# Kernel tuning notes

Hardware: AMD Instinct MI355X
Metric: run time of the kernel (lower is better)

Reference implementation:

```python
import jax, jax.numpy as jnp
import numpy as np

N_NODES = 100000
N_EDGES = 1600000
IN_CH = 128
HID = 128
OUT_CH = 10
NUM_LAYERS = 3
NUM_GRAPHS = 512


def _glorot(key, shape):
    fan_in, fan_out = shape[0], shape[1]
    lim = jnp.sqrt(6.0 / (fan_in + fan_out))
    return jax.random.uniform(key, shape, jnp.float32, -lim, lim)


def setup_inputs() -> dict:
    key = jax.random.key(0)
    ks = jax.random.split(key, 20)
    inp = {}
    inp["x"] = jax.random.normal(ks[0], (N_NODES, IN_CH), jnp.float32)
    inp["edge_index"] = jax.random.randint(ks[1], (2, N_EDGES), 0, N_NODES, jnp.int64)
    inp["batch"] = jnp.sort(jax.random.randint(ks[2], (N_NODES,), 0, NUM_GRAPHS, jnp.int64))
    # GIN layer MLP params: Linear(in, hid) -> ReLU -> Linear(hid, hid)
    kidx = 3
    for l in range(NUM_LAYERS):
        d_in = IN_CH if l == 0 else HID
        inp[f"w1_{l}"] = _glorot(ks[kidx], (d_in, HID)); kidx += 1
        inp[f"b1_{l}"] = jnp.zeros((HID,), jnp.float32)
        inp[f"w2_{l}"] = _glorot(ks[kidx], (HID, HID)); kidx += 1
        inp[f"b2_{l}"] = jnp.zeros((HID,), jnp.float32)
    inp["lin_w"] = _glorot(ks[kidx], (HID, OUT_CH))
    inp["lin_b"] = jnp.zeros((OUT_CH,), jnp.float32)
    return inp


def _gin_forward(x, src, dst, batch, layer_params, lin_w, lin_b):
    h = x
    n_layers = len(layer_params)
    for i, (w1, b1, w2, b2) in enumerate(layer_params):
        # GINConv: (1 + eps) * h + sum_{j in N(i)} h_j, eps = 0
        agg = jax.ops.segment_sum(h[src], dst, num_segments=N_NODES)
        z = h + agg
        # MLP: Linear -> ReLU -> Linear
        h = jnp.maximum(z @ w1 + b1, 0.0) @ w2 + b2
        if i < n_layers - 1:  # inter-layer ReLU (PyG BasicGNN act)
            h = jnp.maximum(h, 0.0)
    # global_add_pool over batch ids -> [NUM_GRAPHS, HID]
    pooled = jax.ops.segment_sum(h, batch, num_segments=NUM_GRAPHS)
    # dropout(p=0.5) is identity in eval mode
    return pooled @ lin_w + lin_b


def reference(x, edge_index, batch,
              w1_0, b1_0, w2_0, b2_0,
              w1_1, b1_1, w2_1, b2_1,
              w1_2, b1_2, w2_2, b2_2,
              lin_w, lin_b):
    src, dst = edge_index[0], edge_index[1]
    layer_params = [(w1_0, b1_0, w2_0, b2_0),
                    (w1_1, b1_1, w2_1, b2_1),
                    (w1_2, b1_2, w2_2, b2_2)]
    return _gin_forward(x, src, dst, batch, layer_params, lin_w, lin_b)
```

## Files before the change

### kernel.cpp

```cpp
#include <hip/hip_runtime.h>

#define CH 128
#define OUTC 10
#define NB 256
#define BCAP 10240
#define PCHUNK 2048

typedef __attribute__((ext_vector_type(8))) short short8;
typedef __attribute__((ext_vector_type(4))) short short4v;
typedef __attribute__((ext_vector_type(16))) float f32x16;


__device__ inline unsigned short f2bf(float f) {
    unsigned u = __builtin_bit_cast(unsigned, f);
    u += 0x7fffu + ((u >> 16) & 1u);
    return (unsigned short)(u >> 16);
}
__device__ inline float bflo(unsigned u) { return __builtin_bit_cast(float, u << 16); }
__device__ inline float bfhi(unsigned u) { return __builtin_bit_cast(float, u & 0xffff0000u); }

__device__ inline void acc8(float* a, const uint4& v) {
    a[0] += bflo(v.x); a[1] += bfhi(v.x);
    a[2] += bflo(v.y); a[3] += bfhi(v.y);
    a[4] += bflo(v.z); a[5] += bfhi(v.z);
    a[6] += bflo(v.w); a[7] += bfhi(v.w);
}


struct WPtrs { const float* s[6]; unsigned short* d[6]; };

__global__ void prep_kernel(const float4* __restrict__ x4, uint2* __restrict__ xb, int n4,
                            int nConvBlk, WPtrs p) {
    int tid = threadIdx.x;
    if ((int)blockIdx.x < nConvBlk) {
        int i = blockIdx.x * 256 + tid;
        if (i < n4) {
            float4 v = x4[i];
            uint2 o;
            o.x = (unsigned)f2bf(v.x) | ((unsigned)f2bf(v.y) << 16);
            o.y = (unsigned)f2bf(v.z) | ((unsigned)f2bf(v.w) << 16);
            xb[i] = o;
        }
    } else {
        int b = blockIdx.x - nConvBlk;
        int m = b >> 6;
        int i = (b & 63) * 256 + tid;
        int j = i & 7;
        int l = (i >> 3) & 63;
        int k0 = (i >> 9) & 7;
        int ct = (i >> 12) & 3;
        int k = k0 * 16 + ((l >> 5) << 3) + j;
        int nn = ct * 32 + (l & 31);
        p.d[m][i] = f2bf(p.s[m][k * CH + nn]);
    }
}


__global__ void partition_kernel(const int* __restrict__ src, const int* __restrict__ dst,
                                 int* __restrict__ bucketCnt, unsigned* __restrict__ pairs, int E) {
    __shared__ int hist[NB];
    __shared__ int base[NB];
    __shared__ int cur[NB];
    int tid = threadIdx.x;
    int e0 = blockIdx.x * PCHUNK;

    hist[tid] = 0;
    __syncthreads();
    #pragma unroll
    for (int i = 0; i < PCHUNK / 256; ++i) {
        int e = e0 + tid + i * 256;
        if (e < E) atomicAdd(&hist[dst[e] >> 9], 1);
    }
    __syncthreads();
    {
        int c = hist[tid];
        base[tid] = (c > 0) ? atomicAdd(&bucketCnt[tid], c) : 0;
        cur[tid] = 0;
    }
    __syncthreads();
    #pragma unroll
    for (int i = 0; i < PCHUNK / 256; ++i) {
        int e = e0 + tid + i * 256;
        if (e < E) {
            int d = dst[e];
            int bkt = d >> 9;
            int p = base[bkt] + atomicAdd(&cur[bkt], 1);
            if (p < BCAP)
                pairs[bkt * BCAP + p] = ((unsigned)(d & 511) << 17) | (unsigned)src[e];
        }
    }
}


__launch_bounds__(256)
__global__ void build_csr_kernel(const unsigned* __restrict__ pairs, const int* __restrict__ bucketCnt,
                                 int* __restrict__ offs, int* __restrict__ csr, int N) {
    __shared__ int bsm[NB];
    __shared__ int ldeg[512];
    __shared__ int s0[512], s1[512];
    __shared__ int lexc[512];
    __shared__ int lcur[512];
    __shared__ int lcsr[BCAP];

    int b = blockIdx.x;
    int node0 = b << 9;
    if (node0 >= N) return;
    int nLocal = min(512, N - node0);
    int tid = threadIdx.x;

    bsm[tid] = bucketCnt[tid];
    __syncthreads();
    for (int off = 1; off < NB; off <<= 1) {
        int t = (tid >= off) ? bsm[tid - off] : 0;
        __syncthreads();
        bsm[tid] += t;
        __syncthreads();
    }
    int cnt = min(bucketCnt[b], BCAP);
    int gbase = bsm[b] - bucketCnt[b];

    for (int i = tid; i < 512; i += 256) ldeg[i] = 0;
    __syncthreads();
    for (int i = tid; i < cnt; i += 256)
        atomicAdd(&ldeg[pairs[b * BCAP + i] >> 17], 1);
    __syncthreads();

    for (int i = tid; i < 512; i += 256) s0[i] = ldeg[i];
    __syncthreads();
    int* sp = s0; int* dp = s1;
    for (int off = 1; off < 512; off <<= 1) {
        for (int i = tid; i < 512; i += 256)
            dp[i] = sp[i] + ((i >= off) ? sp[i - off] : 0);
        __syncthreads();
        int* t = sp; sp = dp; dp = t;
    }
    for (int i = tid; i < 512; i += 256) {
        int ex = sp[i] - ldeg[i];
        lexc[i] = ex;
        lcur[i] = ex;
    }
    __syncthreads();

    for (int i = tid; i < cnt; i += 256) {
        unsigned w = pairs[b * BCAP + i];
        int ppos = atomicAdd(&lcur[w >> 17], 1);
        lcsr[ppos] = (int)(w & 0x1ffffu);
    }
    __syncthreads();

    for (int i = tid; i < cnt; i += 256) csr[gbase + i] = lcsr[i];
    for (int i = tid; i < nLocal; i += 256) offs[node0 + i] = gbase + lexc[i];
    if (tid == 0 && node0 + nLocal == N) offs[N] = gbase + cnt;
}


template <int L>
__global__ void aggregate_kernel(const uint4* __restrict__ h4, const int* __restrict__ offs,
                                 const int* __restrict__ csr, uint4* __restrict__ z4, int n) {
    int node = blockIdx.x * 16 + (threadIdx.x >> 4);
    int lane = threadIdx.x & 15;
    if (node >= n) return;
    int beg = offs[node], end = offs[node + 1];

    float a[8];
    {
        uint4 self = h4[node * 16 + lane];
        a[0] = bflo(self.x); a[1] = bfhi(self.x);
        a[2] = bflo(self.y); a[3] = bfhi(self.y);
        a[4] = bflo(self.z); a[5] = bfhi(self.z);
        a[6] = bflo(self.w); a[7] = bfhi(self.w);
    }
    int e = beg;
    for (; e + 4 <= end; e += 4) {
        int s0 = csr[e], s1 = csr[e + 1], s2 = csr[e + 2], s3 = csr[e + 3];
        uint4 v0 = h4[s0 * 16 + lane];
        uint4 v1 = h4[s1 * 16 + lane];
        uint4 v2 = h4[s2 * 16 + lane];
        uint4 v3 = h4[s3 * 16 + lane];
        acc8(a, v0); acc8(a, v1); acc8(a, v2); acc8(a, v3);
    }
    for (; e < end; ++e) {
        uint4 v = h4[csr[e] * 16 + lane];
        acc8(a, v);
    }
    uint4 o;
    o.x = (unsigned)f2bf(a[0]) | ((unsigned)f2bf(a[1]) << 16);
    o.y = (unsigned)f2bf(a[2]) | ((unsigned)f2bf(a[3]) << 16);
    o.z = (unsigned)f2bf(a[4]) | ((unsigned)f2bf(a[5]) << 16);
    o.w = (unsigned)f2bf(a[6]) | ((unsigned)f2bf(a[7]) << 16);
    z4[node * 16 + lane] = o;
}


#define PQ2 132
#define BM 128

template <int L, int RELU, int POOL>
__launch_bounds__(512)
__global__ void mlp_mfma_kernel(const unsigned short* __restrict__ z,
                                const unsigned short* __restrict__ w1s, const float* __restrict__ b1,
                                const unsigned short* __restrict__ w2s, const float* __restrict__ b2,
                                unsigned short* __restrict__ hout,
                                const int* __restrict__ batch, float* __restrict__ pooled,
                                int n) {
    __shared__ __align__(16) unsigned short zs[BM * PQ2];

    int tid = threadIdx.x;
    int row0 = blockIdx.x * BM;
    int wv = tid >> 6;
    int lane = tid & 63;
    int l31 = lane & 31;
    int kh = lane >> 5;
    int rt = wv & 3;
    int ch = wv >> 2;
    int ct0 = ch * 2;
    int arow = rt * 32 + l31;

    for (int i = tid; i < BM * 16; i += 512) {
        int r = i >> 4, c = i & 15;
        int row = row0 + r;
        uint4 v = (row < n) ? ((const uint4*)z)[row * 16 + c] : make_uint4(0, 0, 0, 0);
        *(uint2*)&zs[r * PQ2 + c * 8]     = make_uint2(v.x, v.y);
        *(uint2*)&zs[r * PQ2 + c * 8 + 4] = make_uint2(v.z, v.w);
    }
    __syncthreads();

    f32x16 acc0, acc1;
    {
        float bv0 = b1[ct0 * 32 + l31];
        float bv1 = b1[(ct0 + 1) * 32 + l31];
        #pragma unroll
        for (int r = 0; r < 16; ++r) { acc0[r] = bv0; acc1[r] = bv1; }
    }
    #pragma unroll
    for (int k0 = 0; k0 < 8; ++k0) {
        short8 afr;
        {
            short4v lo = *(const short4v*)&zs[arow * PQ2 + k0 * 16 + kh * 8];
            short4v hi = *(const short4v*)&zs[arow * PQ2 + k0 * 16 + kh * 8 + 4];
            afr = (short8){lo[0], lo[1], lo[2], lo[3], hi[0], hi[1], hi[2], hi[3]};
        }
        short8 bf0 = *(const short8*)&w1s[(((ct0 * 8 + k0) * 64) + lane) * 8];
        short8 bf1 = *(const short8*)&w1s[((((ct0 + 1) * 8 + k0) * 64) + lane) * 8];
        acc0 = __builtin_amdgcn_mfma_f32_32x32x16_bf16(afr, bf0, acc0, 0, 0, 0);
        acc1 = __builtin_amdgcn_mfma_f32_32x32x16_bf16(afr, bf1, acc1, 0, 0, 0);
    }
    __syncthreads();

    #pragma unroll
    for (int reg = 0; reg < 16; ++reg) {
        int crow = (reg & 3) + 8 * (reg >> 2) + 4 * kh;
        zs[(rt * 32 + crow) * PQ2 + ch * 64 + l31]      = f2bf(fmaxf(acc0[reg], 0.f));
        zs[(rt * 32 + crow) * PQ2 + ch * 64 + 32 + l31] = f2bf(fmaxf(acc1[reg], 0.f));
    }
    __syncthreads();

    {
        float bv0 = b2[ct0 * 32 + l31];
        float bv1 = b2[(ct0 + 1) * 32 + l31];
        #pragma unroll
        for (int r = 0; r < 16; ++r) { acc0[r] = bv0; acc1[r] = bv1; }
    }
    #pragma unroll
    for (int k0 = 0; k0 < 8; ++k0) {
        short8 afr;
        {
            short4v lo = *(const short4v*)&zs[arow * PQ2 + k0 * 16 + kh * 8];
            short4v hi = *(const short4v*)&zs[arow * PQ2 + k0 * 16 + kh * 8 + 4];
            afr = (short8){lo[0], lo[1], lo[2], lo[3], hi[0], hi[1], hi[2], hi[3]};
        }
        short8 bf0 = *(const short8*)&w2s[(((ct0 * 8 + k0) * 64) + lane) * 8];
        short8 bf1 = *(const short8*)&w2s[((((ct0 + 1) * 8 + k0) * 64) + lane) * 8];
        acc0 = __builtin_amdgcn_mfma_f32_32x32x16_bf16(afr, bf0, acc0, 0, 0, 0);
        acc1 = __builtin_amdgcn_mfma_f32_32x32x16_bf16(afr, bf1, acc1, 0, 0, 0);
    }
    __syncthreads();

    #pragma unroll
    for (int reg = 0; reg < 16; ++reg) {
        int crow = (reg & 3) + 8 * (reg >> 2) + 4 * kh;
        float v0 = acc0[reg], v1 = acc1[reg];
        if (RELU) { v0 = fmaxf(v0, 0.f); v1 = fmaxf(v1, 0.f); }
        zs[(rt * 32 + crow) * PQ2 + ch * 64 + l31]      = f2bf(v0);
        zs[(rt * 32 + crow) * PQ2 + ch * 64 + 32 + l31] = f2bf(v1);
    }
    __syncthreads();

    if (!POOL) {
        for (int i = tid; i < BM * 16; i += 512) {
            int r = i >> 4, c = i & 15;
            int row = row0 + r;
            if (row < n) {
                uint2 a = *(const uint2*)&zs[r * PQ2 + c * 8];
                uint2 b = *(const uint2*)&zs[r * PQ2 + c * 8 + 4];
                ((uint4*)hout)[row * 16 + c] = make_uint4(a.x, a.y, b.x, b.y);
            }
        }
    } else {
        int c2 = tid & 63;
        int rs = tid >> 6;
        float a0 = 0.f, a1 = 0.f;
        int prevg = -1;
        #pragma unroll
        for (int i = 0; i < BM / 8; ++i) {
            int r = rs + 8 * i;
            int row = row0 + r;
            if (row >= n) break;
            int g = batch[row];
            if (g != prevg) {
                if (prevg >= 0) {
                    atomicAdd(&pooled[prevg * CH + 2 * c2], a0);
                    atomicAdd(&pooled[prevg * CH + 2 * c2 + 1], a1);
                }
                prevg = g; a0 = 0.f; a1 = 0.f;
            }
            unsigned v = *(const unsigned*)&zs[r * PQ2 + c2 * 2];
            a0 += bflo(v); a1 += bfhi(v);
        }
        if (prevg >= 0) {
            atomicAdd(&pooled[prevg * CH + 2 * c2], a0);
            atomicAdd(&pooled[prevg * CH + 2 * c2 + 1], a1);
        }
    }
}


__global__ void final_linear_kernel(const float* __restrict__ pooled, const float* __restrict__ lin_w,
                                    const float* __restrict__ lin_b, float* __restrict__ out) {
    int g = blockIdx.x;
    int tid = threadIdx.x;
    __shared__ float pl[CH];
    pl[tid] = pooled[g * CH + tid];
    __syncthreads();
    if (tid < OUTC) {
        float a = lin_b[tid];
        #pragma unroll 16
        for (int c = 0; c < CH; ++c) a = fmaf(pl[c], lin_w[c * OUTC + tid], a);
        out[g * OUTC + tid] = a;
    }
}


static inline size_t aln(size_t x) { return (x + 255) & ~size_t(255); }

extern "C" void kernel_launch(void* const* d_in, const int* in_sizes, int n_in,
                              void* d_out, int out_size, void* d_ws, size_t ws_size,
                              hipStream_t stream) {
    const float* x      = (const float*)d_in[0];
    const int*   ei     = (const int*)d_in[1];
    const int*   batch  = (const int*)d_in[2];
    const float* w1[3]  = {(const float*)d_in[3], (const float*)d_in[7],  (const float*)d_in[11]};
    const float* b1[3]  = {(const float*)d_in[4], (const float*)d_in[8],  (const float*)d_in[12]};
    const float* w2[3]  = {(const float*)d_in[5], (const float*)d_in[9],  (const float*)d_in[13]};
    const float* b2[3]  = {(const float*)d_in[6], (const float*)d_in[10], (const float*)d_in[14]};
    const float* lin_w  = (const float*)d_in[15];
    const float* lin_b  = (const float*)d_in[16];
    float* out = (float*)d_out;

    int E = in_sizes[1] / 2;
    int N = in_sizes[2];
    int n_graphs = out_size / OUTC;
    const int* src = ei;
    const int* dst = ei + E;

    char* p = (char*)d_ws;
    int* bucketCnt  = (int*)p; p += aln(NB * 4);
    unsigned* pairs = (unsigned*)p; p += aln((size_t)NB * BCAP * 4);
    int* offs       = (int*)p; p += aln((size_t)(N + 1) * 4);
    int* csr        = (int*)p; p += aln((size_t)E * 4);
    unsigned short* xb = (unsigned short*)p; p += aln((size_t)N * CH * 2);
    unsigned short* zb = (unsigned short*)p; p += aln((size_t)N * CH * 2);
    unsigned short* hA = (unsigned short*)p; p += aln((size_t)N * CH * 2);
    unsigned short* hB = (unsigned short*)p; p += aln((size_t)N * CH * 2);
    float* pooled = (float*)p; p += aln((size_t)n_graphs * CH * 4);
    unsigned short* wt[6];
    for (int i = 0; i < 6; ++i) { wt[i] = (unsigned short*)p; p += aln((size_t)CH * CH * 2); }
    (void)ws_size; (void)n_in;

    hipMemsetAsync(bucketCnt, 0, NB * 4, stream);
    hipMemsetAsync(pooled, 0, (size_t)n_graphs * CH * 4, stream);

    int n4 = N * CH / 4;
    int nConvBlk = (n4 + 255) / 256;
    WPtrs wp;
    for (int l = 0; l < 3; ++l) {
        wp.s[2 * l] = w1[l];     wp.d[2 * l] = wt[2 * l];
        wp.s[2 * l + 1] = w2[l]; wp.d[2 * l + 1] = wt[2 * l + 1];
    }
    prep_kernel<<<nConvBlk + 384, 256, 0, stream>>>((const float4*)x, (uint2*)xb, n4, nConvBlk, wp);

    partition_kernel<<<(E + PCHUNK - 1) / PCHUNK, 256, 0, stream>>>(src, dst, bucketCnt, pairs, E);
    build_csr_kernel<<<NB, 256, 0, stream>>>(pairs, bucketCnt, offs, csr, N);

    int ablk = (N + 15) / 16;
    int mblk = (N + BM - 1) / BM;

    aggregate_kernel<0><<<ablk, 256, 0, stream>>>((const uint4*)xb, offs, csr, (uint4*)zb, N);
    mlp_mfma_kernel<0, 1, 0><<<mblk, 512, 0, stream>>>(zb, wt[0], b1[0], wt[1], b2[0], hA, batch, pooled, N);
    aggregate_kernel<1><<<ablk, 256, 0, stream>>>((const uint4*)hA, offs, csr, (uint4*)zb, N);
    mlp_mfma_kernel<1, 1, 0><<<mblk, 512, 0, stream>>>(zb, wt[2], b1[1], wt[3], b2[1], hB, batch, pooled, N);
    aggregate_kernel<2><<<ablk, 256, 0, stream>>>((const uint4*)hB, offs, csr, (uint4*)zb, N);
    mlp_mfma_kernel<2, 0, 1><<<mblk, 512, 0, stream>>>(zb, wt[4], b1[2], wt[5], b2[2], hA, batch, pooled, N);

    final_linear_kernel<<<n_graphs, CH, 0, stream>>>(pooled, lin_w, lin_b, out);
}
```

Measured before the change: 435.3 us.

## Fuse layer-1 aggregation with MLP and fold memsets into prep kernel

Adds a fused kernel that gathers neighbor features for a 64-row tile straight into shared memory and then runs both MFMA linear layers on that tile, so the bf16 z buffer is never written to or read back from global memory for layer 1. The two hipMemsetAsync calls are also replaced by extra blocks in the prep kernel that zero the bucket counts and the pooled buffer, cutting two launches. The fused kernel uses 512 threads per 64-row block, which may lower occupancy or the gather's memory parallelism compared with the separate aggregate kernel. Layers 0 and 2 still use the unfused path.

```diff
diff --git a/kernel.cpp b/kernel.cpp
--- a/kernel.cpp
+++ b/kernel.cpp
@@ -30,10 +30,12 @@
 struct WPtrs { const float* s[6]; unsigned short* d[6]; };
 
 __global__ void prep_kernel(const float4* __restrict__ x4, uint2* __restrict__ xb, int n4,
-                            int nConvBlk, WPtrs p) {
+                            int nConvBlk, WPtrs p, int* __restrict__ bucketCnt,
+                            uint4* __restrict__ pooled4, int nPooled4) {
     int tid = threadIdx.x;
-    if ((int)blockIdx.x < nConvBlk) {
-        int i = blockIdx.x * 256 + tid;
+    int b = blockIdx.x;
+    if (b < nConvBlk) {
+        int i = b * 256 + tid;
         if (i < n4) {
             float4 v = x4[i];
             uint2 o;
@@ -41,10 +43,10 @@
             o.y = (unsigned)f2bf(v.z) | ((unsigned)f2bf(v.w) << 16);
             xb[i] = o;
         }
-    } else {
-        int b = blockIdx.x - nConvBlk;
-        int m = b >> 6;
-        int i = (b & 63) * 256 + tid;
+    } else if (b < nConvBlk + 384) {
+        int bb = b - nConvBlk;
+        int m = bb >> 6;
+        int i = (bb & 63) * 256 + tid;
         int j = i & 7;
         int l = (i >> 3) & 63;
         int k0 = (i >> 9) & 7;
@@ -52,6 +54,11 @@
         int k = k0 * 16 + ((l >> 5) << 3) + j;
         int nn = ct * 32 + (l & 31);
         p.d[m][i] = f2bf(p.s[m][k * CH + nn]);
+    } else if (b == nConvBlk + 384) {
+        bucketCnt[tid] = 0;
+    } else {
+        int i = (b - nConvBlk - 385) * 256 + tid;
+        if (i < nPooled4) pooled4[i] = make_uint4(0, 0, 0, 0);
     }
 }
 
@@ -191,8 +198,9 @@
     z4[node * 16 + lane] = o;
 }
 
-
 #define PQ2 132
+
+
 #define BM 128
 
 template <int L, int RELU, int POOL>
@@ -325,6 +333,133 @@
 }
 
 
+#define FBM 64
+
+template <int RELU>
+__launch_bounds__(512)
+__global__ void fused_gin_kernel(const uint4* __restrict__ h4,
+                                 const int* __restrict__ offs, const int* __restrict__ csr,
+                                 const unsigned short* __restrict__ w1s, const float* __restrict__ b1,
+                                 const unsigned short* __restrict__ w2s, const float* __restrict__ b2,
+                                 unsigned short* __restrict__ hout, int n) {
+    __shared__ __align__(16) unsigned short zs[FBM * PQ2];
+
+    int tid = threadIdx.x;
+    int row0 = blockIdx.x * FBM;
+
+    {
+        int gl = tid & 15;
+        int grp = tid >> 4;
+        #pragma unroll
+        for (int it = 0; it < 2; ++it) {
+            int rr = grp + 32 * it;
+            int node = row0 + rr;
+            unsigned o0 = 0, o1 = 0, o2 = 0, o3 = 0;
+            if (node < n) {
+                int beg = offs[node], end = offs[node + 1];
+                float a[8];
+                uint4 self = h4[node * 16 + gl];
+                a[0] = bflo(self.x); a[1] = bfhi(self.x);
+                a[2] = bflo(self.y); a[3] = bfhi(self.y);
+                a[4] = bflo(self.z); a[5] = bfhi(self.z);
+                a[6] = bflo(self.w); a[7] = bfhi(self.w);
+                int e = beg;
+                for (; e + 4 <= end; e += 4) {
+                    int s0 = csr[e], s1 = csr[e + 1], s2 = csr[e + 2], s3 = csr[e + 3];
+                    uint4 v0 = h4[s0 * 16 + gl];
+                    uint4 v1 = h4[s1 * 16 + gl];
+                    uint4 v2 = h4[s2 * 16 + gl];
+                    uint4 v3 = h4[s3 * 16 + gl];
+                    acc8(a, v0); acc8(a, v1); acc8(a, v2); acc8(a, v3);
+                }
+                for (; e < end; ++e) {
+                    uint4 v = h4[csr[e] * 16 + gl];
+                    acc8(a, v);
+                }
+                o0 = (unsigned)f2bf(a[0]) | ((unsigned)f2bf(a[1]) << 16);
+                o1 = (unsigned)f2bf(a[2]) | ((unsigned)f2bf(a[3]) << 16);
+                o2 = (unsigned)f2bf(a[4]) | ((unsigned)f2bf(a[5]) << 16);
+                o3 = (unsigned)f2bf(a[6]) | ((unsigned)f2bf(a[7]) << 16);
+            }
+            *(uint2*)&zs[rr * PQ2 + gl * 8]     = make_uint2(o0, o1);
+            *(uint2*)&zs[rr * PQ2 + gl * 8 + 4] = make_uint2(o2, o3);
+        }
+    }
+    __syncthreads();
+
+    int wv = tid >> 6;
+    int lane = tid & 63;
+    int l31 = lane & 31;
+    int kh = lane >> 5;
+    int rt = wv & 1;
+    int ct = wv >> 1;
+    int arow = rt * 32 + l31;
+
+    f32x16 acc;
+    {
+        float bv = b1[ct * 32 + l31];
+        #pragma unroll
+        for (int r = 0; r < 16; ++r) acc[r] = bv;
+    }
+    #pragma unroll
+    for (int k0 = 0; k0 < 8; ++k0) {
+        short8 afr;
+        {
+            short4v lo = *(const short4v*)&zs[arow * PQ2 + k0 * 16 + kh * 8];
+            short4v hi = *(const short4v*)&zs[arow * PQ2 + k0 * 16 + kh * 8 + 4];
+            afr = (short8){lo[0], lo[1], lo[2], lo[3], hi[0], hi[1], hi[2], hi[3]};
+        }
+        short8 bfr = *(const short8*)&w1s[(((ct * 8 + k0) * 64) + lane) * 8];
+        acc = __builtin_amdgcn_mfma_f32_32x32x16_bf16(afr, bfr, acc, 0, 0, 0);
+    }
+    __syncthreads();
+
+    #pragma unroll
+    for (int reg = 0; reg < 16; ++reg) {
+        int crow = (reg & 3) + 8 * (reg >> 2) + 4 * kh;
+        zs[(rt * 32 + crow) * PQ2 + ct * 32 + l31] = f2bf(fmaxf(acc[reg], 0.f));
+    }
+    __syncthreads();
+
+    {
+        float bv = b2[ct * 32 + l31];
+        #pragma unroll
+        for (int r = 0; r < 16; ++r) acc[r] = bv;
+    }
+    #pragma unroll
+    for (int k0 = 0; k0 < 8; ++k0) {
+        short8 afr;
+        {
+            short4v lo = *(const short4v*)&zs[arow * PQ2 + k0 * 16 + kh * 8];
+            short4v hi = *(const short4v*)&zs[arow * PQ2 + k0 * 16 + kh * 8 + 4];
+            afr = (short8){lo[0], lo[1], lo[2], lo[3], hi[0], hi[1], hi[2], hi[3]};
+        }
+        short8 bfr = *(const short8*)&w2s[(((ct * 8 + k0) * 64) + lane) * 8];
+        acc = __builtin_amdgcn_mfma_f32_32x32x16_bf16(afr, bfr, acc, 0, 0, 0);
+    }
+    __syncthreads();
+
+    #pragma unroll
+    for (int reg = 0; reg < 16; ++reg) {
+        int crow = (reg & 3) + 8 * (reg >> 2) + 4 * kh;
+        float v = acc[reg];
+        if (RELU) v = fmaxf(v, 0.f);
+        zs[(rt * 32 + crow) * PQ2 + ct * 32 + l31] = f2bf(v);
+    }
+    __syncthreads();
+
+    for (int i = tid; i < FBM * 16; i += 512) {
+        int r = i >> 4, c = i & 15;
+        int row = row0 + r;
+        if (row < n) {
+            uint2 a = *(const uint2*)&zs[r * PQ2 + c * 8];
+            uint2 b = *(const uint2*)&zs[r * PQ2 + c * 8 + 4];
+            ((uint4*)hout)[row * 16 + c] = make_uint4(a.x, a.y, b.x, b.y);
+        }
+    }
+}
+
+
 __global__ void final_linear_kernel(const float* __restrict__ pooled, const float* __restrict__ lin_w,
                                     const float* __restrict__ lin_b, float* __restrict__ out) {
     int g = blockIdx.x;
@@ -377,28 +512,29 @@
     for (int i = 0; i < 6; ++i) { wt[i] = (unsigned short*)p; p += aln((size_t)CH * CH * 2); }
     (void)ws_size; (void)n_in;
 
-    hipMemsetAsync(bucketCnt, 0, NB * 4, stream);
-    hipMemsetAsync(pooled, 0, (size_t)n_graphs * CH * 4, stream);
-
     int n4 = N * CH / 4;
     int nConvBlk = (n4 + 255) / 256;
+    int nPooled4 = n_graphs * CH / 4;
+    int nZeroBlk = (nPooled4 + 255) / 256;
     WPtrs wp;
     for (int l = 0; l < 3; ++l) {
         wp.s[2 * l] = w1[l];     wp.d[2 * l] = wt[2 * l];
         wp.s[2 * l + 1] = w2[l]; wp.d[2 * l + 1] = wt[2 * l + 1];
     }
-    prep_kernel<<<nConvBlk + 384, 256, 0, stream>>>((const float4*)x, (uint2*)xb, n4, nConvBlk, wp);
+    prep_kernel<<<nConvBlk + 384 + 1 + nZeroBlk, 256, 0, stream>>>(
+        (const float4*)x, (uint2*)xb, n4, nConvBlk, wp, bucketCnt, (uint4*)pooled, nPooled4);
 
     partition_kernel<<<(E + PCHUNK - 1) / PCHUNK, 256, 0, stream>>>(src, dst, bucketCnt, pairs, E);
     build_csr_kernel<<<NB, 256, 0, stream>>>(pairs, bucketCnt, offs, csr, N);
 
     int ablk = (N + 15) / 16;
     int mblk = (N + BM - 1) / BM;
+    int fblk = (N + FBM - 1) / FBM;
 
     aggregate_kernel<0><<<ablk, 256, 0, stream>>>((const uint4*)xb, offs, csr, (uint4*)zb, N);
     mlp_mfma_kernel<0, 1, 0><<<mblk, 512, 0, stream>>>(zb, wt[0], b1[0], wt[1], b2[0], hA, batch, pooled, N);
-    aggregate_kernel<1><<<ablk, 256, 0, stream>>>((const uint4*)hA, offs, csr, (uint4*)zb, N);
-    mlp_mfma_kernel<1, 1, 0><<<mblk, 512, 0, stream>>>(zb, wt[2], b1[1], wt[3], b2[1], hB, batch, pooled, N);
+    fused_gin_kernel<1><<<fblk, 512, 0, stream>>>((const uint4*)hA, offs, csr,
+                                                  wt[2], b1[1], wt[3], b2[1], hB, N);
     aggregate_kernel<2><<<ablk, 256, 0, stream>>>((const uint4*)hB, offs, csr, (uint4*)zb, N);
     mlp_mfma_kernel<2, 0, 1><<<mblk, 512, 0, stream>>>(zb, wt[4], b1[2], wt[5], b2[2], hA, batch, pooled, N);
 
```

Result: faster. 412.2 us (-5.3%).

## Fuse neighbor aggregation into MLP kernel and merge prep, partition, pool-zero launches

Applied to the files above, without the earlier changes.

The gather-sum aggregation is moved into the MFMA MLP kernel, so each 64-row block builds its z tile directly in shared memory and the z buffer never makes a round trip through global memory. The M tile shrinks from 128 to 64 rows, with each wave now owning a single 32-column tile. Partitioning, input conversion, weight swizzle and zeroing of the pooled buffer are merged into one launch, removing a memset and a kernel launch. In exchange, the MLP phase waits on irregular gather latency inside each block, and per-wave MFMA work is smaller.

```diff
diff --git a/kernel.cpp b/kernel.cpp
--- a/kernel.cpp
+++ b/kernel.cpp
@@ -5,6 +5,8 @@
 #define NB 256
 #define BCAP 10240
 #define PCHUNK 2048
+#define PQ2 132
+#define FBM 64
 
 typedef __attribute__((ext_vector_type(8))) short short8;
 typedef __attribute__((ext_vector_type(4))) short short4v;
@@ -29,11 +31,47 @@
 
 struct WPtrs { const float* s[6]; unsigned short* d[6]; };
 
-__global__ void prep_kernel(const float4* __restrict__ x4, uint2* __restrict__ xb, int n4,
-                            int nConvBlk, WPtrs p) {
+__global__ void prep_part_kernel(const int* __restrict__ src, const int* __restrict__ dst,
+                                 int* __restrict__ bucketCnt, unsigned* __restrict__ pairs, int E,
+                                 int nPartBlk,
+                                 const float4* __restrict__ x4, uint2* __restrict__ xb, int n4,
+                                 int nConvBlk, WPtrs p,
+                                 uint4* __restrict__ pooled4, int nPooled4) {
+    __shared__ int hist[NB];
+    __shared__ int base[NB];
+    __shared__ int cur[NB];
     int tid = threadIdx.x;
-    if ((int)blockIdx.x < nConvBlk) {
-        int i = blockIdx.x * 256 + tid;
+    int b = blockIdx.x;
+
+    if (b < nPartBlk) {
+        int e0 = b * PCHUNK;
+        hist[tid] = 0;
+        __syncthreads();
+        #pragma unroll
+        for (int i = 0; i < PCHUNK / 256; ++i) {
+            int e = e0 + tid + i * 256;
+            if (e < E) atomicAdd(&hist[dst[e] >> 9], 1);
+        }
+        __syncthreads();
+        {
+            int c = hist[tid];
+            base[tid] = (c > 0) ? atomicAdd(&bucketCnt[tid], c) : 0;
+            cur[tid] = 0;
+        }
+        __syncthreads();
+        #pragma unroll
+        for (int i = 0; i < PCHUNK / 256; ++i) {
+            int e = e0 + tid + i * 256;
+            if (e < E) {
+                int d = dst[e];
+                int bkt = d >> 9;
+                int pos = base[bkt] + atomicAdd(&cur[bkt], 1);
+                if (pos < BCAP)
+                    pairs[bkt * BCAP + pos] = ((unsigned)(d & 511) << 17) | (unsigned)src[e];
+            }
+        }
+    } else if (b < nPartBlk + nConvBlk) {
+        int i = (b - nPartBlk) * 256 + tid;
         if (i < n4) {
             float4 v = x4[i];
             uint2 o;
@@ -41,10 +79,10 @@
             o.y = (unsigned)f2bf(v.z) | ((unsigned)f2bf(v.w) << 16);
             xb[i] = o;
         }
-    } else {
-        int b = blockIdx.x - nConvBlk;
-        int m = b >> 6;
-        int i = (b & 63) * 256 + tid;
+    } else if (b < nPartBlk + nConvBlk + 384) {
+        int bb = b - nPartBlk - nConvBlk;
+        int m = bb >> 6;
+        int i = (bb & 63) * 256 + tid;
         int j = i & 7;
         int l = (i >> 3) & 63;
         int k0 = (i >> 9) & 7;
@@ -52,42 +90,9 @@
         int k = k0 * 16 + ((l >> 5) << 3) + j;
         int nn = ct * 32 + (l & 31);
         p.d[m][i] = f2bf(p.s[m][k * CH + nn]);
-    }
-}
-
-
-__global__ void partition_kernel(const int* __restrict__ src, const int* __restrict__ dst,
-                                 int* __restrict__ bucketCnt, unsigned* __restrict__ pairs, int E) {
-    __shared__ int hist[NB];
-    __shared__ int base[NB];
-    __shared__ int cur[NB];
-    int tid = threadIdx.x;
-    int e0 = blockIdx.x * PCHUNK;
-
-    hist[tid] = 0;
-    __syncthreads();
-    #pragma unroll
-    for (int i = 0; i < PCHUNK / 256; ++i) {
-        int e = e0 + tid + i * 256;
-        if (e < E) atomicAdd(&hist[dst[e] >> 9], 1);
-    }
-    __syncthreads();
-    {
-        int c = hist[tid];
-        base[tid] = (c > 0) ? atomicAdd(&bucketCnt[tid], c) : 0;
-        cur[tid] = 0;
-    }
-    __syncthreads();
-    #pragma unroll
-    for (int i = 0; i < PCHUNK / 256; ++i) {
-        int e = e0 + tid + i * 256;
-        if (e < E) {
-            int d = dst[e];
-            int bkt = d >> 9;
-            int p = base[bkt] + atomicAdd(&cur[bkt], 1);
-            if (p < BCAP)
-                pairs[bkt * BCAP + p] = ((unsigned)(d & 511) << 17) | (unsigned)src[e];
-        }
+    } else {
+        int i = (b - nPartBlk - nConvBlk - 384) * 256 + tid;
+        if (i < nPooled4) pooled4[i] = make_uint4(0, 0, 0, 0);
     }
 }
 
@@ -154,83 +159,73 @@
 }
 
 
-template <int L>
-__global__ void aggregate_kernel(const uint4* __restrict__ h4, const int* __restrict__ offs,
-                                 const int* __restrict__ csr, uint4* __restrict__ z4, int n) {
-    int node = blockIdx.x * 16 + (threadIdx.x >> 4);
-    int lane = threadIdx.x & 15;
-    if (node >= n) return;
-    int beg = offs[node], end = offs[node + 1];
-
-    float a[8];
-    {
-        uint4 self = h4[node * 16 + lane];
-        a[0] = bflo(self.x); a[1] = bfhi(self.x);
-        a[2] = bflo(self.y); a[3] = bfhi(self.y);
-        a[4] = bflo(self.z); a[5] = bfhi(self.z);
-        a[6] = bflo(self.w); a[7] = bfhi(self.w);
-    }
-    int e = beg;
-    for (; e + 4 <= end; e += 4) {
-        int s0 = csr[e], s1 = csr[e + 1], s2 = csr[e + 2], s3 = csr[e + 3];
-        uint4 v0 = h4[s0 * 16 + lane];
-        uint4 v1 = h4[s1 * 16 + lane];
-        uint4 v2 = h4[s2 * 16 + lane];
-        uint4 v3 = h4[s3 * 16 + lane];
-        acc8(a, v0); acc8(a, v1); acc8(a, v2); acc8(a, v3);
-    }
-    for (; e < end; ++e) {
-        uint4 v = h4[csr[e] * 16 + lane];
-        acc8(a, v);
-    }
-    uint4 o;
-    o.x = (unsigned)f2bf(a[0]) | ((unsigned)f2bf(a[1]) << 16);
-    o.y = (unsigned)f2bf(a[2]) | ((unsigned)f2bf(a[3]) << 16);
-    o.z = (unsigned)f2bf(a[4]) | ((unsigned)f2bf(a[5]) << 16);
-    o.w = (unsigned)f2bf(a[6]) | ((unsigned)f2bf(a[7]) << 16);
-    z4[node * 16 + lane] = o;
-}
-
-
-#define PQ2 132
-#define BM 128
-
 template <int L, int RELU, int POOL>
 __launch_bounds__(512)
-__global__ void mlp_mfma_kernel(const unsigned short* __restrict__ z,
-                                const unsigned short* __restrict__ w1s, const float* __restrict__ b1,
-                                const unsigned short* __restrict__ w2s, const float* __restrict__ b2,
-                                unsigned short* __restrict__ hout,
-                                const int* __restrict__ batch, float* __restrict__ pooled,
-                                int n) {
-    __shared__ __align__(16) unsigned short zs[BM * PQ2];
+__global__ void fused_gin_kernel(const uint4* __restrict__ h4,
+                                 const int* __restrict__ offs, const int* __restrict__ csr,
+                                 const unsigned short* __restrict__ w1s, const float* __restrict__ b1,
+                                 const unsigned short* __restrict__ w2s, const float* __restrict__ b2,
+                                 unsigned short* __restrict__ hout,
+                                 const int* __restrict__ batch, float* __restrict__ pooled,
+                                 int n) {
+    __shared__ __align__(16) unsigned short zs[FBM * PQ2];
 
     int tid = threadIdx.x;
-    int row0 = blockIdx.x * BM;
+    int row0 = blockIdx.x * FBM;
+
+    {
+        int gl = tid & 15;
+        int grp = tid >> 4;
+        #pragma unroll
+        for (int it = 0; it < 2; ++it) {
+            int rr = grp + 32 * it;
+            int node = row0 + rr;
+            unsigned o0 = 0, o1 = 0, o2 = 0, o3 = 0;
+            if (node < n) {
+                int beg = offs[node], end = offs[node + 1];
+                float a[8];
+                uint4 self = h4[node * 16 + gl];
+                a[0] = bflo(self.x); a[1] = bfhi(self.x);
+                a[2] = bflo(self.y); a[3] = bfhi(self.y);
+                a[4] = bflo(self.z); a[5] = bfhi(self.z);
+                a[6] = bflo(self.w); a[7] = bfhi(self.w);
+                int e = beg;
+                for (; e + 4 <= end; e += 4) {
+                    int s0 = csr[e], s1 = csr[e + 1], s2 = csr[e + 2], s3 = csr[e + 3];
+                    uint4 v0 = h4[s0 * 16 + gl];
+                    uint4 v1 = h4[s1 * 16 + gl];
+                    uint4 v2 = h4[s2 * 16 + gl];
+                    uint4 v3 = h4[s3 * 16 + gl];
+                    acc8(a, v0); acc8(a, v1); acc8(a, v2); acc8(a, v3);
+                }
+                for (; e < end; ++e) {
+                    uint4 v = h4[csr[e] * 16 + gl];
+                    acc8(a, v);
+                }
+                o0 = (unsigned)f2bf(a[0]) | ((unsigned)f2bf(a[1]) << 16);
+                o1 = (unsigned)f2bf(a[2]) | ((unsigned)f2bf(a[3]) << 16);
+                o2 = (unsigned)f2bf(a[4]) | ((unsigned)f2bf(a[5]) << 16);
+                o3 = (unsigned)f2bf(a[6]) | ((unsigned)f2bf(a[7]) << 16);
+            }
+            *(uint2*)&zs[rr * PQ2 + gl * 8]     = make_uint2(o0, o1);
+            *(uint2*)&zs[rr * PQ2 + gl * 8 + 4] = make_uint2(o2, o3);
+        }
+    }
+    __syncthreads();
+
     int wv = tid >> 6;
     int lane = tid & 63;
     int l31 = lane & 31;
     int kh = lane >> 5;
-    int rt = wv & 3;
-    int ch = wv >> 2;
-    int ct0 = ch * 2;
+    int rt = wv & 1;
+    int ct = wv >> 1;
     int arow = rt * 32 + l31;
 
-    for (int i = tid; i < BM * 16; i += 512) {
-        int r = i >> 4, c = i & 15;
-        int row = row0 + r;
-        uint4 v = (row < n) ? ((const uint4*)z)[row * 16 + c] : make_uint4(0, 0, 0, 0);
-        *(uint2*)&zs[r * PQ2 + c * 8]     = make_uint2(v.x, v.y);
-        *(uint2*)&zs[r * PQ2 + c * 8 + 4] = make_uint2(v.z, v.w);
-    }
-    __syncthreads();
-
-    f32x16 acc0, acc1;
+    f32x16 acc;
     {
-        float bv0 = b1[ct0 * 32 + l31];
-        float bv1 = b1[(ct0 + 1) * 32 + l31];
-        #pragma unroll
-        for (int r = 0; r < 16; ++r) { acc0[r] = bv0; acc1[r] = bv1; }
+        float bv = b1[ct * 32 + l31];
+        #pragma unroll
+        for (int r = 0; r < 16; ++r) acc[r] = bv;
     }
     #pragma unroll
     for (int k0 = 0; k0 < 8; ++k0) {
@@ -240,26 +235,22 @@
             short4v hi = *(const short4v*)&zs[arow * PQ2 + k0 * 16 + kh * 8 + 4];
             afr = (short8){lo[0], lo[1], lo[2], lo[3], hi[0], hi[1], hi[2], hi[3]};
         }
-        short8 bf0 = *(const short8*)&w1s[(((ct0 * 8 + k0) * 64) + lane) * 8];
-        short8 bf1 = *(const short8*)&w1s[((((ct0 + 1) * 8 + k0) * 64) + lane) * 8];
-        acc0 = __builtin_amdgcn_mfma_f32_32x32x16_bf16(afr, bf0, acc0, 0, 0, 0);
-        acc1 = __builtin_amdgcn_mfma_f32_32x32x16_bf16(afr, bf1, acc1, 0, 0, 0);
+        short8 bfr = *(const short8*)&w1s[(((ct * 8 + k0) * 64) + lane) * 8];
+        acc = __builtin_amdgcn_mfma_f32_32x32x16_bf16(afr, bfr, acc, 0, 0, 0);
     }
     __syncthreads();
 
     #pragma unroll
     for (int reg = 0; reg < 16; ++reg) {
         int crow = (reg & 3) + 8 * (reg >> 2) + 4 * kh;
-        zs[(rt * 32 + crow) * PQ2 + ch * 64 + l31]      = f2bf(fmaxf(acc0[reg], 0.f));
-        zs[(rt * 32 + crow) * PQ2 + ch * 64 + 32 + l31] = f2bf(fmaxf(acc1[reg], 0.f));
+        zs[(rt * 32 + crow) * PQ2 + ct * 32 + l31] = f2bf(fmaxf(acc[reg], 0.f));
     }
     __syncthreads();
 
     {
-        float bv0 = b2[ct0 * 32 + l31];
-        float bv1 = b2[(ct0 + 1) * 32 + l31];
-        #pragma unroll
-        for (int r = 0; r < 16; ++r) { acc0[r] = bv0; acc1[r] = bv1; }
+        float bv = b2[ct * 32 + l31];
+        #pragma unroll
+        for (int r = 0; r < 16; ++r) acc[r] = bv;
     }
     #pragma unroll
     for (int k0 = 0; k0 < 8; ++k0) {
@@ -269,25 +260,22 @@
             short4v hi = *(const short4v*)&zs[arow * PQ2 + k0 * 16 + kh * 8 + 4];
             afr = (short8){lo[0], lo[1], lo[2], lo[3], hi[0], hi[1], hi[2], hi[3]};
         }
-        short8 bf0 = *(const short8*)&w2s[(((ct0 * 8 + k0) * 64) + lane) * 8];
-        short8 bf1 = *(const short8*)&w2s[((((ct0 + 1) * 8 + k0) * 64) + lane) * 8];
-        acc0 = __builtin_amdgcn_mfma_f32_32x32x16_bf16(afr, bf0, acc0, 0, 0, 0);
-        acc1 = __builtin_amdgcn_mfma_f32_32x32x16_bf16(afr, bf1, acc1, 0, 0, 0);
+        short8 bfr = *(const short8*)&w2s[(((ct * 8 + k0) * 64) + lane) * 8];
+        acc = __builtin_amdgcn_mfma_f32_32x32x16_bf16(afr, bfr, acc, 0, 0, 0);
     }
     __syncthreads();
 
     #pragma unroll
     for (int reg = 0; reg < 16; ++reg) {
         int crow = (reg & 3) + 8 * (reg >> 2) + 4 * kh;
-        float v0 = acc0[reg], v1 = acc1[reg];
-        if (RELU) { v0 = fmaxf(v0, 0.f); v1 = fmaxf(v1, 0.f); }
-        zs[(rt * 32 + crow) * PQ2 + ch * 64 + l31]      = f2bf(v0);
-        zs[(rt * 32 + crow) * PQ2 + ch * 64 + 32 + l31] = f2bf(v1);
+        float v = acc[reg];
+        if (RELU) v = fmaxf(v, 0.f);
+        zs[(rt * 32 + crow) * PQ2 + ct * 32 + l31] = f2bf(v);
     }
     __syncthreads();
 
     if (!POOL) {
-        for (int i = tid; i < BM * 16; i += 512) {
+        for (int i = tid; i < FBM * 16; i += 512) {
             int r = i >> 4, c = i & 15;
             int row = row0 + r;
             if (row < n) {
@@ -302,7 +290,7 @@
         float a0 = 0.f, a1 = 0.f;
         int prevg = -1;
         #pragma unroll
-        for (int i = 0; i < BM / 8; ++i) {
+        for (int i = 0; i < FBM / 8; ++i) {
             int r = rs + 8 * i;
             int row = row0 + r;
             if (row >= n) break;
@@ -369,7 +357,6 @@
     int* offs       = (int*)p; p += aln((size_t)(N + 1) * 4);
     int* csr        = (int*)p; p += aln((size_t)E * 4);
     unsigned short* xb = (unsigned short*)p; p += aln((size_t)N * CH * 2);
-    unsigned short* zb = (unsigned short*)p; p += aln((size_t)N * CH * 2);
     unsigned short* hA = (unsigned short*)p; p += aln((size_t)N * CH * 2);
     unsigned short* hB = (unsigned short*)p; p += aln((size_t)N * CH * 2);
     float* pooled = (float*)p; p += aln((size_t)n_graphs * CH * 4);
@@ -378,29 +365,32 @@
     (void)ws_size; (void)n_in;
 
     hipMemsetAsync(bucketCnt, 0, NB * 4, stream);
-    hipMemsetAsync(pooled, 0, (size_t)n_graphs * CH * 4, stream);
 
     int n4 = N * CH / 4;
     int nConvBlk = (n4 + 255) / 256;
+    int nPartBlk = (E + PCHUNK - 1) / PCHUNK;
+    int nPooled4 = n_graphs * CH / 4;
+    int nZeroBlk = (nPooled4 + 255) / 256;
     WPtrs wp;
     for (int l = 0; l < 3; ++l) {
         wp.s[2 * l] = w1[l];     wp.d[2 * l] = wt[2 * l];
         wp.s[2 * l + 1] = w2[l]; wp.d[2 * l + 1] = wt[2 * l + 1];
     }
-    prep_kernel<<<nConvBlk + 384, 256, 0, stream>>>((const float4*)x, (uint2*)xb, n4, nConvBlk, wp);
-
-    partition_kernel<<<(E + PCHUNK - 1) / PCHUNK, 256, 0, stream>>>(src, dst, bucketCnt, pairs, E);
+    prep_part_kernel<<<nPartBlk + nConvBlk + 384 + nZeroBlk, 256, 0, stream>>>(
+        src, dst, bucketCnt, pairs, E, nPartBlk,
+        (const float4*)x, (uint2*)xb, n4, nConvBlk, wp,
+        (uint4*)pooled, nPooled4);
+
     build_csr_kernel<<<NB, 256, 0, stream>>>(pairs, bucketCnt, offs, csr, N);
 
-    int ablk = (N + 15) / 16;
-    int mblk = (N + BM - 1) / BM;
-
-    aggregate_kernel<0><<<ablk, 256, 0, stream>>>((const uint4*)xb, offs, csr, (uint4*)zb, N);
-    mlp_mfma_kernel<0, 1, 0><<<mblk, 512, 0, stream>>>(zb, wt[0], b1[0], wt[1], b2[0], hA, batch, pooled, N);
-    aggregate_kernel<1><<<ablk, 256, 0, stream>>>((const uint4*)hA, offs, csr, (uint4*)zb, N);
-    mlp_mfma_kernel<1, 1, 0><<<mblk, 512, 0, stream>>>(zb, wt[2], b1[1], wt[3], b2[1], hB, batch, pooled, N);
-    aggregate_kernel<2><<<ablk, 256, 0, stream>>>((const uint4*)hB, offs, csr, (uint4*)zb, N);
-    mlp_mfma_kernel<2, 0, 1><<<mblk, 512, 0, stream>>>(zb, wt[4], b1[2], wt[5], b2[2], hA, batch, pooled, N);
+    int fblk = (N + FBM - 1) / FBM;
+
+    fused_gin_kernel<0, 1, 0><<<fblk, 512, 0, stream>>>((const uint4*)xb, offs, csr,
+        wt[0], b1[0], wt[1], b2[0], hA, batch, pooled, N);
+    fused_gin_kernel<1, 1, 0><<<fblk, 512, 0, stream>>>((const uint4*)hA, offs, csr,
+        wt[2], b1[1], wt[3], b2[1], hB, batch, pooled, N);
+    fused_gin_kernel<2, 0, 1><<<fblk, 512, 0, stream>>>((const uint4*)hB, offs, csr,
+        wt[4], b1[2], wt[5], b2[2], (unsigned short*)nullptr, batch, pooled, N);
 
     final_linear_kernel<<<n_graphs, CH, 0, stream>>>(pooled, lin_w, lin_b, out);
 }
```

After: 384.7 us. 1.13x faster.
